# Optimization experiments

Hardware: AMD Instinct MI355X
Metric: run time of the kernel (lower is better)

Reference implementation:

```python
import jax, jax.numpy as jnp
import numpy as np

N_NODES = 50000
N_EDGES = 800000
DIM_IN = 128
DIM_H = 128
DIM_OUT = 10
N_GRAPHS = 256


def _glorot(key, shape):
    lim = float(np.sqrt(6.0 / (shape[0] + shape[1])))
    return jax.random.uniform(key, shape, jnp.float32, -lim, lim)


def setup_inputs() -> dict:
    key = jax.random.key(0)
    ks = jax.random.split(key, 8)
    x = jax.random.normal(ks[0], (N_NODES, DIM_IN), jnp.float32)
    edge_index = jax.random.randint(ks[1], (2, N_EDGES), 0, N_NODES, dtype=jnp.int64)
    batch = jnp.sort(jax.random.randint(ks[2], (N_NODES,), 0, N_GRAPHS, dtype=jnp.int64))
    return {
        'x': x,
        'edge_index': edge_index,
        'batch': batch,
        'W1': _glorot(ks[3], (DIM_IN, DIM_H)),
        'b1': jnp.zeros((DIM_H,), jnp.float32),
        'W2': _glorot(ks[4], (DIM_H, DIM_H)),
        'b2': jnp.zeros((DIM_H,), jnp.float32),
        'Wl1': _glorot(ks[5], (2 * DIM_H, 2 * DIM_H)),
        'bl1': jnp.zeros((2 * DIM_H,), jnp.float32),
        'Wl2': _glorot(ks[6], (2 * DIM_H, DIM_OUT)),
        'bl2': jnp.zeros((DIM_OUT,), jnp.float32),
    }


def _gcn_conv(h, W, b, src, dst, norm, n):
    # x @ W, gather source rows, scale by symmetric norm, scatter-add to dest
    m = (h @ W)[src] * norm[:, None]          # [E+N, dim_h]
    return jax.ops.segment_sum(m, dst, num_segments=n) + b


def reference(x, edge_index, batch, W1, b1, W2, b2, Wl1, bl1, Wl2, bl2):
    n = x.shape[0]
    loops = jnp.arange(n, dtype=edge_index.dtype)
    src = jnp.concatenate([edge_index[0], loops])  # add self-loops (PyG GCNConv default)
    dst = jnp.concatenate([edge_index[1], loops])
    deg = jax.ops.segment_sum(jnp.ones_like(dst, x.dtype), dst, num_segments=n)
    dinv = jnp.where(deg > 0, jax.lax.rsqrt(jnp.maximum(deg, 1.0)), 0.0)
    norm = dinv[src] * dinv[dst]
    # eval mode: dropout is identity
    h1 = _gcn_conv(x, W1, b1, src, dst, norm, n)
    h2 = _gcn_conv(h1, W2, b2, src, dst, norm, n)
    g1 = jax.ops.segment_sum(h1, batch, num_segments=N_GRAPHS)  # global_add_pool
    g2 = jax.ops.segment_sum(h2, batch, num_segments=N_GRAPHS)
    g = jnp.concatenate([g1, g2], axis=1)  # [N_GRAPHS, 2*dim_h]
    h = jax.nn.relu(g @ Wl1 + bl1)
    h = h @ Wl2 + bl2
    return (h, jax.nn.log_softmax(h, axis=1))
```

## Files before the change

### kernel.cpp

```cpp
#include <hip/hip_runtime.h>
#include <hip/hip_bf16.h>
#include <math.h>


#define DIMH 128
#define EBCAP 8192
#define SCAT_CHUNK 2048

typedef __attribute__((ext_vector_type(8))) short s16x8;
typedef __attribute__((ext_vector_type(4))) float f32x4;

__device__ inline ushort f2b(float f) {
    uint u = __float_as_uint(f);
    return (ushort)((u + 0x7fffu + ((u >> 16) & 1u)) >> 16);
}
__device__ inline uint pack2(float lo, float hi) {
    return (uint)f2b(lo) | ((uint)f2b(hi) << 16);
}
__device__ inline float blo(uint u) { return __uint_as_float(u << 16); }
__device__ inline float bhi(uint u) { return __uint_as_float(u & 0xffff0000u); }

__global__ __launch_bounds__(256) void k_front(const int* __restrict__ src,
                                               const int* __restrict__ dst,
                                               int* __restrict__ bcnt,
                                               uint* __restrict__ ebuf, int E, int scnb,
                                               const float* __restrict__ x,
                                               ushort* __restrict__ Xb, int n8, int cvnb,
                                               const float* __restrict__ W1,
                                               const float* __restrict__ W2,
                                               ushort* __restrict__ WT1,
                                               ushort* __restrict__ WT2) {
    __shared__ int h[4][256];
    __shared__ int wb[4][256];
    int blk = blockIdx.x;
    int t = threadIdx.x;
    if (blk < scnb) {
        int wave = t >> 6;
        h[0][t] = 0; h[1][t] = 0; h[2][t] = 0; h[3][t] = 0;
        __syncthreads();
        int e0 = blk * SCAT_CHUNK;
        int e1 = e0 + SCAT_CHUNK; if (e1 > E) e1 = E;
        for (int e = e0 + t; e < e1; e += 256)
            atomicAdd(&h[wave][dst[e] >> 8], 1);
        __syncthreads();
        {
            int h0 = h[0][t], h1 = h[1][t], h2 = h[2][t], h3 = h[3][t];
            int tot = h0 + h1 + h2 + h3;
            int gb = tot ? atomicAdd(&bcnt[t], tot) : 0;
            wb[0][t] = gb;
            wb[1][t] = gb + h0;
            wb[2][t] = gb + h0 + h1;
            wb[3][t] = gb + h0 + h1 + h2;
            h[0][t] = 0; h[1][t] = 0; h[2][t] = 0; h[3][t] = 0;
        }
        __syncthreads();
        for (int e = e0 + t; e < e1; e += 256) {
            int d = dst[e];
            int bk = d >> 8;
            int rank = wb[wave][bk] + atomicAdd(&h[wave][bk], 1);
            if (rank < EBCAP)
                ebuf[(size_t)bk * EBCAP + rank] = ((uint)(d & 255) << 24) | (uint)src[e];
        }
    } else if (blk < scnb + cvnb) {
        int i = (blk - scnb) * 256 + t;
        if (i < n8) {
            const float4* in4 = (const float4*)x;
            float4 a = in4[2 * i], b = in4[2 * i + 1];
            uint4 o;
            o.x = pack2(a.x, a.y); o.y = pack2(a.z, a.w);
            o.z = pack2(b.x, b.y); o.w = pack2(b.z, b.w);
            *(uint4*)(Xb + (size_t)i * 8) = o;
        }
    } else {
        int idx = (blk - scnb - cvnb) * 256 + t;
        const float* W = (idx < 16384) ? W1 : W2;
        ushort* WT = (idx < 16384) ? WT1 : WT2;
        int tt = idx & 16383;
        int k = tt >> 7, nn = tt & 127;
        WT[nn * 128 + k] = f2b(W[tt]);
    }
}

__global__ __launch_bounds__(256) void k_bcsr(const uint* __restrict__ ebuf,
                                              const int* __restrict__ bcnt,
                                              float* __restrict__ dinv,
                                              int2* __restrict__ rng,
                                              int* __restrict__ srt, int n) {
    __shared__ int cnt[256];
    __shared__ int wsum[4];
    __shared__ int stage[EBCAP];
    int b = blockIdx.x;
    int t = threadIdx.x;
    int c = bcnt[b]; if (c > EBCAP) c = EBCAP;
    size_t B = (size_t)b * EBCAP;
    cnt[t] = 0;
    __syncthreads();
    for (int i = t; i < c; i += 256)
        atomicAdd(&cnt[ebuf[B + i] >> 24], 1);
    __syncthreads();
    int v = cnt[t];
    int incl = v;
    for (int k = 1; k < 64; k <<= 1) {
        int u = __shfl_up(incl, k, 64);
        if ((t & 63) >= k) incl += u;
    }
    if ((t & 63) == 63) wsum[t >> 6] = incl;
    __syncthreads();
    int add = 0;
    for (int j = 0; j < (t >> 6); ++j) add += wsum[j];
    incl += add;
    int loc = incl - v;
    int node = b * 256 + t;
    if (node < n) {
        dinv[node] = rsqrtf((float)(v + 1));
        rng[node] = make_int2((int)B + loc, (int)B + loc + v);
    }
    cnt[t] = loc;
    __syncthreads();
    for (int i = t; i < c; i += 256) {
        uint r = ebuf[B + i];
        int p = atomicAdd(&cnt[r >> 24], 1);
        stage[p] = (int)(r & 0xffffffu);
    }
    __syncthreads();
    for (int i = t; i < c; i += 256) srt[B + i] = stage[i];
}

__device__ __forceinline__ void gemm_body(const ushort* __restrict__ Xb,
                                          const ushort* __restrict__ WT,
                                          const float* __restrict__ scale,
                                          ushort* __restrict__ P, int n,
                                          int blk, ushort* lds) {
    ushort* Xs = lds;
    ushort* Ws = lds + 64 * 128;
    const int tid = threadIdx.x;
    const int row0 = blk * 64;
    for (int ci = tid; ci < 1024; ci += 256) {
        int r = ci >> 4, c16 = ci & 15;
        uint dstB = (uint)(r * 256 + c16 * 16) ^ (uint)((r & 7) << 4);
        uint4 v = make_uint4(0u, 0u, 0u, 0u);
        if (row0 + r < n) v = *(const uint4*)(Xb + (size_t)(row0 + r) * 128 + c16 * 8);
        *(uint4*)((char*)Xs + dstB) = v;
    }
    for (int ci = tid; ci < 2048; ci += 256) {
        int r = ci >> 4, c16 = ci & 15;
        uint dstB = (uint)(r * 256 + c16 * 16) ^ (uint)((r & 7) << 4);
        *(uint4*)((char*)Ws + dstB) = *(const uint4*)(WT + (size_t)r * 128 + c16 * 8);
    }
    __syncthreads();
    const int wave = tid >> 6, lane = tid & 63;
    const int l15 = lane & 15, g = lane >> 4;
    f32x4 acc[8];
#pragma unroll
    for (int nt = 0; nt < 8; ++nt) acc[nt] = (f32x4){0.f, 0.f, 0.f, 0.f};
    const int tr = wave * 16 + l15;
    const uint aswz = (uint)((tr & 7) << 4);
#pragma unroll
    for (int kk = 0; kk < 4; ++kk) {
        uint aB = ((uint)(tr * 256 + kk * 64 + g * 16)) ^ aswz;
        s16x8 afrag = *(const s16x8*)((const char*)Xs + aB);
#pragma unroll
        for (int nt = 0; nt < 8; ++nt) {
            int wr = nt * 16 + l15;
            uint bB = ((uint)(wr * 256 + kk * 64 + g * 16)) ^ ((uint)((wr & 7) << 4));
            s16x8 bfrag = *(const s16x8*)((const char*)Ws + bB);
            acc[nt] = __builtin_amdgcn_mfma_f32_16x16x32_bf16(afrag, bfrag, acc[nt], 0, 0, 0);
        }
    }
    float sc[4];
#pragma unroll
    for (int reg = 0; reg < 4; ++reg) {
        int grow = row0 + wave * 16 + g * 4 + reg;
        sc[reg] = (grow < n) ? scale[grow] : 0.f;
    }
#pragma unroll
    for (int nt = 0; nt < 8; ++nt) {
        int gcol = nt * 16 + l15;
#pragma unroll
        for (int reg = 0; reg < 4; ++reg) {
            int grow = row0 + wave * 16 + g * 4 + reg;
            if (grow < n) P[(size_t)grow * 128 + gcol] = f2b(sc[reg] * acc[nt][reg]);
        }
    }
}

__global__ __launch_bounds__(256) void k_gemm(const ushort* __restrict__ Xb,
                                              const ushort* __restrict__ WT,
                                              const float* __restrict__ scale,
                                              ushort* __restrict__ P, int n) {
    __shared__ ushort lds[64 * 128 + 128 * 128];
    gemm_body(Xb, WT, scale, P, n, blockIdx.x, lds);
}

__device__ __forceinline__ void pool_body(const ushort* __restrict__ Hb,
                                          const int* __restrict__ batch,
                                          float* __restrict__ Gpart, int n,
                                          int blk, int* range, float* part) {
    int g = blk >> 2, q = blk & 3;
    if (threadIdx.x < 2) {
        int target = g + threadIdx.x;
        int lo = 0, hi = n;
        while (lo < hi) { int m = (lo + hi) >> 1; if (batch[m] < target) lo = m + 1; else hi = m; }
        range[threadIdx.x] = lo;
    }
    __syncthreads();
    int c = threadIdx.x & 127, h = threadIdx.x >> 7;
    int r = range[0] + q * 2 + h, r1 = range[1];
    float s0 = 0.f, s1 = 0.f;
    for (; r + 8 < r1; r += 16) {
        s0 += __uint_as_float((uint)Hb[(size_t)r       * 128 + c] << 16);
        s1 += __uint_as_float((uint)Hb[(size_t)(r + 8) * 128 + c] << 16);
    }
    for (; r < r1; r += 8) s0 += __uint_as_float((uint)Hb[(size_t)r * 128 + c] << 16);
    part[threadIdx.x] = s0 + s1;
    __syncthreads();
    if (threadIdx.x < 128)
        Gpart[(size_t)blk * 128 + threadIdx.x] = part[threadIdx.x] + part[threadIdx.x + 128];
}

__global__ __launch_bounds__(256) void k_mid(const ushort* __restrict__ Hb,
                                             const ushort* __restrict__ WT,
                                             const float* __restrict__ scale,
                                             ushort* __restrict__ P, int n, int gemnb,
                                             const int* __restrict__ batch,
                                             float* __restrict__ Gpart) {
    __shared__ ushort lds[64 * 128 + 128 * 128];
    __shared__ int range[2];
    __shared__ float part[256];
    int blk = blockIdx.x;
    if (blk < gemnb) {
        gemm_body(Hb, WT, scale, P, n, blk, lds);
    } else {
        pool_body(Hb, batch, Gpart, n, blk - gemnb, range, part);
    }
}

__global__ __launch_bounds__(256) void k_aggregate(const ushort* __restrict__ Pb,
                                                   const int2* __restrict__ rng,
                                                   const int* __restrict__ srt,
                                                   const float* __restrict__ dinv,
                                                   const float* __restrict__ bias,
                                                   ushort* __restrict__ Hb, int n) {
    int wave = threadIdx.x >> 6;
    int lane = threadIdx.x & 63;
    int i = blockIdx.x * 4 + wave;
    if (i >= n) return;
    int q   = lane >> 4;
    int sub = lane & 15;
    const uint4* P4 = (const uint4*)Pb;
    float a0 = 0.f, a1 = 0.f, a2 = 0.f, a3 = 0.f;
    float a4 = 0.f, a5 = 0.f, a6 = 0.f, a7 = 0.f;
    if (q == 0) {
        uint4 u = P4[(size_t)i * 16 + sub];
        a0 = blo(u.x); a1 = bhi(u.x); a2 = blo(u.y); a3 = bhi(u.y);
        a4 = blo(u.z); a5 = bhi(u.z); a6 = blo(u.w); a7 = bhi(u.w);
    }
    int2 r2 = rng[i];
    int e1 = r2.y;
    int e  = r2.x + q;
    while (e + 12 < e1) {
        int s0 = srt[e], s1 = srt[e + 4], s2 = srt[e + 8], s3 = srt[e + 12];
        uint4 u0 = P4[(size_t)s0 * 16 + sub];
        uint4 u1 = P4[(size_t)s1 * 16 + sub];
        uint4 u2 = P4[(size_t)s2 * 16 + sub];
        uint4 u3 = P4[(size_t)s3 * 16 + sub];
        a0 += (blo(u0.x) + blo(u1.x)) + (blo(u2.x) + blo(u3.x));
        a1 += (bhi(u0.x) + bhi(u1.x)) + (bhi(u2.x) + bhi(u3.x));
        a2 += (blo(u0.y) + blo(u1.y)) + (blo(u2.y) + blo(u3.y));
        a3 += (bhi(u0.y) + bhi(u1.y)) + (bhi(u2.y) + bhi(u3.y));
        a4 += (blo(u0.z) + blo(u1.z)) + (blo(u2.z) + blo(u3.z));
        a5 += (bhi(u0.z) + bhi(u1.z)) + (bhi(u2.z) + bhi(u3.z));
        a6 += (blo(u0.w) + blo(u1.w)) + (blo(u2.w) + blo(u3.w));
        a7 += (bhi(u0.w) + bhi(u1.w)) + (bhi(u2.w) + bhi(u3.w));
        e += 16;
    }
    while (e < e1) {
        uint4 u = P4[(size_t)srt[e] * 16 + sub];
        a0 += blo(u.x); a1 += bhi(u.x); a2 += blo(u.y); a3 += bhi(u.y);
        a4 += blo(u.z); a5 += bhi(u.z); a6 += blo(u.w); a7 += bhi(u.w);
        e += 4;
    }
    a0 += __shfl_xor(a0, 16, 64); a0 += __shfl_xor(a0, 32, 64);
    a1 += __shfl_xor(a1, 16, 64); a1 += __shfl_xor(a1, 32, 64);
    a2 += __shfl_xor(a2, 16, 64); a2 += __shfl_xor(a2, 32, 64);
    a3 += __shfl_xor(a3, 16, 64); a3 += __shfl_xor(a3, 32, 64);
    a4 += __shfl_xor(a4, 16, 64); a4 += __shfl_xor(a4, 32, 64);
    a5 += __shfl_xor(a5, 16, 64); a5 += __shfl_xor(a5, 32, 64);
    a6 += __shfl_xor(a6, 16, 64); a6 += __shfl_xor(a6, 32, 64);
    a7 += __shfl_xor(a7, 16, 64); a7 += __shfl_xor(a7, 32, 64);
    if (q == 0) {
        float di = dinv[i];
        int c = sub * 8;
        float4 b0 = *(const float4*)(bias + c);
        float4 b1 = *(const float4*)(bias + c + 4);
        uint4 o;
        o.x = pack2(fmaf(di, a0, b0.x), fmaf(di, a1, b0.y));
        o.y = pack2(fmaf(di, a2, b0.z), fmaf(di, a3, b0.w));
        o.z = pack2(fmaf(di, a4, b1.x), fmaf(di, a5, b1.y));
        o.w = pack2(fmaf(di, a6, b1.z), fmaf(di, a7, b1.w));
        *(uint4*)(Hb + (size_t)i * 128 + c) = o;
    }
}

__global__ __launch_bounds__(256) void k_mlp(const float* __restrict__ Gp1,
                                             const ushort* __restrict__ Hb,
                                             const int* __restrict__ batch, int n,
                                             const float* __restrict__ Wl1,
                                             const float* __restrict__ bl1,
                                             const float* __restrict__ Wl2,
                                             const float* __restrict__ bl2,
                                             float* __restrict__ out) {
    __shared__ float gs[256];
    __shared__ float zs[256];
    __shared__ float part[256];
    __shared__ float l[10];
    __shared__ int range[2];
    int g = blockIdx.x, j = threadIdx.x;
    if (j < 2) {
        int target = g + j;
        int lo = 0, hi = n;
        while (lo < hi) { int m = (lo + hi) >> 1; if (batch[m] < target) lo = m + 1; else hi = m; }
        range[j] = lo;
    }
    __syncthreads();
    {
        int c = j & 127, h = j >> 7;
        int r = range[0] + h, r1 = range[1];
        float s0 = 0.f, s1 = 0.f, s2 = 0.f, s3 = 0.f;
        for (; r + 6 < r1; r += 8) {
            s0 += __uint_as_float((uint)Hb[(size_t)r       * 128 + c] << 16);
            s1 += __uint_as_float((uint)Hb[(size_t)(r + 2) * 128 + c] << 16);
            s2 += __uint_as_float((uint)Hb[(size_t)(r + 4) * 128 + c] << 16);
            s3 += __uint_as_float((uint)Hb[(size_t)(r + 6) * 128 + c] << 16);
        }
        for (; r < r1; r += 2) s0 += __uint_as_float((uint)Hb[(size_t)r * 128 + c] << 16);
        part[j] = (s0 + s1) + (s2 + s3);
    }
    __syncthreads();
    if (j < 128) {
        const float* p = Gp1 + (size_t)g * 512 + j;
        gs[j] = (p[0] + p[128]) + (p[256] + p[384]);
        gs[128 + j] = part[j] + part[j + 128];
    }
    __syncthreads();
    float acc = bl1[j];
    for (int k = 0; k < 256; ++k) acc = fmaf(gs[k], Wl1[k * 256 + j], acc);
    zs[j] = fmaxf(acc, 0.f);
    __syncthreads();
    if (j < 10) {
        float a = bl2[j];
        for (int k = 0; k < 256; ++k) a = fmaf(zs[k], Wl2[k * 10 + j], a);
        l[j] = a;
    }
    __syncthreads();
    if (j < 10) {
        float m = l[0];
        for (int i = 1; i < 10; ++i) m = fmaxf(m, l[i]);
        float s = 0.f;
        for (int i = 0; i < 10; ++i) s += expf(l[i] - m);
        float lse = m + logf(s);
        out[g * 10 + j] = l[j];
        out[2560 + g * 10 + j] = l[j] - lse;
    }
}

static inline size_t alignup(size_t v) { return (v + 255) & ~(size_t)255; }

extern "C" void kernel_launch(void* const* d_in, const int* in_sizes, int n_in,
                              void* d_out, int out_size, void* d_ws, size_t ws_size,
                              hipStream_t stream) {
    const float* x    = (const float*)d_in[0];
    const int*   edge = (const int*)d_in[1];
    const int*   batch= (const int*)d_in[2];
    const float* W1   = (const float*)d_in[3];
    const float* b1   = (const float*)d_in[4];
    const float* W2   = (const float*)d_in[5];
    const float* b2   = (const float*)d_in[6];
    const float* Wl1  = (const float*)d_in[7];
    const float* bl1  = (const float*)d_in[8];
    const float* Wl2  = (const float*)d_in[9];
    const float* bl2  = (const float*)d_in[10];

    const int N = in_sizes[2];
    const int E = in_sizes[1] / 2;
    const int* srcIdx = edge;
    const int* dstIdx = edge + E;

    const int nb = (N + 255) >> 8;

    char* ws = (char*)d_ws;
    ushort* Xb    = (ushort*)ws; ws += alignup((size_t)N * DIMH * 2);
    ushort* P     = (ushort*)ws; ws += alignup((size_t)N * DIMH * 2);
    ushort* Hb    = (ushort*)ws; ws += alignup((size_t)N * DIMH * 2);
    ushort* WT1   = (ushort*)ws; ws += alignup((size_t)128 * 128 * 2);
    ushort* WT2   = (ushort*)ws; ws += alignup((size_t)128 * 128 * 2);
    float*  dinv  = (float*)ws;  ws += alignup((size_t)N * 4);
    int2*   rng   = (int2*)ws;   ws += alignup((size_t)N * 8);
    int*    srt   = (int*)ws;    ws += alignup((size_t)nb * EBCAP * 4);
    uint*   ebuf  = (uint*)ws;   ws += alignup((size_t)nb * EBCAP * 4);
    int*    bcnt  = (int*)ws;    ws += alignup((size_t)256 * 4);
    float*  Gp1   = (float*)ws;  ws += alignup((size_t)1024 * 128 * 4);

    const int scnb  = (E + SCAT_CHUNK - 1) / SCAT_CHUNK;
    const int n8    = N * DIMH / 8;
    const int cvnb  = (n8 + 255) / 256;
    const int gemnb = (N + 63) / 64;
    const int aggnb = (N + 3) / 4;

    hipMemsetAsync(bcnt, 0, (size_t)256 * 4, stream);
    k_front<<<scnb + cvnb + 128, 256, 0, stream>>>(srcIdx, dstIdx, bcnt, ebuf, E, scnb,
                                                   x, Xb, n8, cvnb, W1, W2, WT1, WT2);
    k_bcsr<<<nb, 256, 0, stream>>>(ebuf, bcnt, dinv, rng, srt, N);
    k_gemm<<<gemnb, 256, 0, stream>>>(Xb, WT1, dinv, P, N);
    k_aggregate<<<aggnb, 256, 0, stream>>>(P, rng, srt, dinv, b1, Hb, N);
    k_mid<<<gemnb + 1024, 256, 0, stream>>>(Hb, WT2, dinv, P, N, gemnb, batch, Gp1);
    k_aggregate<<<aggnb, 256, 0, stream>>>(P, rng, srt, dinv, b2, Hb, N);
    k_mlp<<<256, 256, 0, stream>>>(Gp1, Hb, batch, N, Wl1, bl1, Wl2, bl2, (float*)d_out);
}
```

Before: 179.6 us.

## Fuse x conversion into first GEMM and merge it with CSR build kernel

The separate fp32-to-bf16 conversion of x is removed, and the first GEMM now reads fp32 x directly and packs it into LDS. Because the GEMM no longer applies the source-side dinv scale, it can run in the same launch as the CSR-building blocks, cutting one kernel launch and one full pass over a bf16 copy of x. In exchange, the aggregation now gathers dinv[src] per edge and multiplies it in with FMAs, which adds scattered 4-byte loads to the edge loop.

```diff
diff --git a/kernel.cpp b/kernel.cpp
--- a/kernel.cpp
+++ b/kernel.cpp
@@ -24,8 +24,6 @@
                                                const int* __restrict__ dst,
                                                int* __restrict__ bcnt,
                                                uint* __restrict__ ebuf, int E, int scnb,
-                                               const float* __restrict__ x,
-                                               ushort* __restrict__ Xb, int n8, int cvnb,
                                                const float* __restrict__ W1,
                                                const float* __restrict__ W2,
                                                ushort* __restrict__ WT1,
@@ -61,18 +59,8 @@
             if (rank < EBCAP)
                 ebuf[(size_t)bk * EBCAP + rank] = ((uint)(d & 255) << 24) | (uint)src[e];
         }
-    } else if (blk < scnb + cvnb) {
-        int i = (blk - scnb) * 256 + t;
-        if (i < n8) {
-            const float4* in4 = (const float4*)x;
-            float4 a = in4[2 * i], b = in4[2 * i + 1];
-            uint4 o;
-            o.x = pack2(a.x, a.y); o.y = pack2(a.z, a.w);
-            o.z = pack2(b.x, b.y); o.w = pack2(b.z, b.w);
-            *(uint4*)(Xb + (size_t)i * 8) = o;
-        }
     } else {
-        int idx = (blk - scnb - cvnb) * 256 + t;
+        int idx = (blk - scnb) * 256 + t;
         const float* W = (idx < 16384) ? W1 : W2;
         ushort* WT = (idx < 16384) ? WT1 : WT2;
         int tt = idx & 16383;
@@ -81,15 +69,12 @@
     }
 }
 
-__global__ __launch_bounds__(256) void k_bcsr(const uint* __restrict__ ebuf,
-                                              const int* __restrict__ bcnt,
-                                              float* __restrict__ dinv,
-                                              int2* __restrict__ rng,
-                                              int* __restrict__ srt, int n) {
-    __shared__ int cnt[256];
-    __shared__ int wsum[4];
-    __shared__ int stage[EBCAP];
-    int b = blockIdx.x;
+__device__ __forceinline__ void bcsr_body(const uint* __restrict__ ebuf,
+                                          const int* __restrict__ bcnt,
+                                          float* __restrict__ dinv,
+                                          int2* __restrict__ rng,
+                                          int* __restrict__ srt, int n,
+                                          int b, int* cnt, int* wsum, int* stage) {
     int t = threadIdx.x;
     int c = bcnt[b]; if (c > EBCAP) c = EBCAP;
     size_t B = (size_t)b * EBCAP;
@@ -126,21 +111,36 @@
     for (int i = t; i < c; i += 256) srt[B + i] = stage[i];
 }
 
-__device__ __forceinline__ void gemm_body(const ushort* __restrict__ Xb,
+template<bool F32IN>
+__device__ __forceinline__ void gemm_body(const void* __restrict__ Xin,
                                           const ushort* __restrict__ WT,
-                                          const float* __restrict__ scale,
                                           ushort* __restrict__ P, int n,
                                           int blk, ushort* lds) {
     ushort* Xs = lds;
     ushort* Ws = lds + 64 * 128;
     const int tid = threadIdx.x;
     const int row0 = blk * 64;
-    for (int ci = tid; ci < 1024; ci += 256) {
-        int r = ci >> 4, c16 = ci & 15;
-        uint dstB = (uint)(r * 256 + c16 * 16) ^ (uint)((r & 7) << 4);
-        uint4 v = make_uint4(0u, 0u, 0u, 0u);
-        if (row0 + r < n) v = *(const uint4*)(Xb + (size_t)(row0 + r) * 128 + c16 * 8);
-        *(uint4*)((char*)Xs + dstB) = v;
+    if (F32IN) {
+        const float* Xf = (const float*)Xin;
+        for (int ci = tid; ci < 2048; ci += 256) {
+            int r = ci >> 5, c8 = ci & 31;
+            uint dstB = (uint)(r * 256 + c8 * 8) ^ (uint)((r & 7) << 4);
+            uint2 v = make_uint2(0u, 0u);
+            if (row0 + r < n) {
+                float4 f = *(const float4*)(Xf + (size_t)(row0 + r) * 128 + c8 * 4);
+                v.x = pack2(f.x, f.y); v.y = pack2(f.z, f.w);
+            }
+            *(uint2*)((char*)Xs + dstB) = v;
+        }
+    } else {
+        const ushort* Xb = (const ushort*)Xin;
+        for (int ci = tid; ci < 1024; ci += 256) {
+            int r = ci >> 4, c16 = ci & 15;
+            uint dstB = (uint)(r * 256 + c16 * 16) ^ (uint)((r & 7) << 4);
+            uint4 v = make_uint4(0u, 0u, 0u, 0u);
+            if (row0 + r < n) v = *(const uint4*)(Xb + (size_t)(row0 + r) * 128 + c16 * 8);
+            *(uint4*)((char*)Xs + dstB) = v;
+        }
     }
     for (int ci = tid; ci < 2048; ci += 256) {
         int r = ci >> 4, c16 = ci & 15;
@@ -167,29 +167,35 @@
             acc[nt] = __builtin_amdgcn_mfma_f32_16x16x32_bf16(afrag, bfrag, acc[nt], 0, 0, 0);
         }
     }
-    float sc[4];
-#pragma unroll
-    for (int reg = 0; reg < 4; ++reg) {
-        int grow = row0 + wave * 16 + g * 4 + reg;
-        sc[reg] = (grow < n) ? scale[grow] : 0.f;
-    }
 #pragma unroll
     for (int nt = 0; nt < 8; ++nt) {
         int gcol = nt * 16 + l15;
 #pragma unroll
         for (int reg = 0; reg < 4; ++reg) {
             int grow = row0 + wave * 16 + g * 4 + reg;
-            if (grow < n) P[(size_t)grow * 128 + gcol] = f2b(sc[reg] * acc[nt][reg]);
-        }
-    }
-}
-
-__global__ __launch_bounds__(256) void k_gemm(const ushort* __restrict__ Xb,
-                                              const ushort* __restrict__ WT,
-                                              const float* __restrict__ scale,
-                                              ushort* __restrict__ P, int n) {
+            if (grow < n) P[(size_t)grow * 128 + gcol] = f2b(acc[nt][reg]);
+        }
+    }
+}
+
+__global__ __launch_bounds__(256) void k_g1csr(const float* __restrict__ x,
+                                               const ushort* __restrict__ WT1,
+                                               ushort* __restrict__ P, int n, int gemnb,
+                                               const uint* __restrict__ ebuf,
+                                               const int* __restrict__ bcnt,
+                                               float* __restrict__ dinv,
+                                               int2* __restrict__ rng,
+                                               int* __restrict__ srt) {
     __shared__ ushort lds[64 * 128 + 128 * 128];
-    gemm_body(Xb, WT, scale, P, n, blockIdx.x, lds);
+    int blk = blockIdx.x;
+    if (blk < gemnb) {
+        gemm_body<true>(x, WT1, P, n, blk, lds);
+    } else {
+        int* cnt   = (int*)lds;
+        int* wsum  = cnt + 256;
+        int* stage = wsum + 8;
+        bcsr_body(ebuf, bcnt, dinv, rng, srt, n, blk - gemnb, cnt, wsum, stage);
+    }
 }
 
 __device__ __forceinline__ void pool_body(const ushort* __restrict__ Hb,
@@ -220,7 +226,6 @@
 
 __global__ __launch_bounds__(256) void k_mid(const ushort* __restrict__ Hb,
                                              const ushort* __restrict__ WT,
-                                             const float* __restrict__ scale,
                                              ushort* __restrict__ P, int n, int gemnb,
                                              const int* __restrict__ batch,
                                              float* __restrict__ Gpart) {
@@ -229,7 +234,7 @@
     __shared__ float part[256];
     int blk = blockIdx.x;
     if (blk < gemnb) {
-        gemm_body(Hb, WT, scale, P, n, blk, lds);
+        gemm_body<false>(Hb, WT, P, n, blk, lds);
     } else {
         pool_body(Hb, batch, Gpart, n, blk - gemnb, range, part);
     }
@@ -248,36 +253,42 @@
     int q   = lane >> 4;
     int sub = lane & 15;
     const uint4* P4 = (const uint4*)Pb;
+    float di = dinv[i];
     float a0 = 0.f, a1 = 0.f, a2 = 0.f, a3 = 0.f;
     float a4 = 0.f, a5 = 0.f, a6 = 0.f, a7 = 0.f;
     if (q == 0) {
         uint4 u = P4[(size_t)i * 16 + sub];
-        a0 = blo(u.x); a1 = bhi(u.x); a2 = blo(u.y); a3 = bhi(u.y);
-        a4 = blo(u.z); a5 = bhi(u.z); a6 = blo(u.w); a7 = bhi(u.w);
+        a0 = di * blo(u.x); a1 = di * bhi(u.x); a2 = di * blo(u.y); a3 = di * bhi(u.y);
+        a4 = di * blo(u.z); a5 = di * bhi(u.z); a6 = di * blo(u.w); a7 = di * bhi(u.w);
     }
     int2 r2 = rng[i];
     int e1 = r2.y;
     int e  = r2.x + q;
     while (e + 12 < e1) {
         int s0 = srt[e], s1 = srt[e + 4], s2 = srt[e + 8], s3 = srt[e + 12];
+        float d0 = dinv[s0], d1 = dinv[s1], d2 = dinv[s2], d3 = dinv[s3];
         uint4 u0 = P4[(size_t)s0 * 16 + sub];
         uint4 u1 = P4[(size_t)s1 * 16 + sub];
         uint4 u2 = P4[(size_t)s2 * 16 + sub];
         uint4 u3 = P4[(size_t)s3 * 16 + sub];
-        a0 += (blo(u0.x) + blo(u1.x)) + (blo(u2.x) + blo(u3.x));
-        a1 += (bhi(u0.x) + bhi(u1.x)) + (bhi(u2.x) + bhi(u3.x));
-        a2 += (blo(u0.y) + blo(u1.y)) + (blo(u2.y) + blo(u3.y));
-        a3 += (bhi(u0.y) + bhi(u1.y)) + (bhi(u2.y) + bhi(u3.y));
-        a4 += (blo(u0.z) + blo(u1.z)) + (blo(u2.z) + blo(u3.z));
-        a5 += (bhi(u0.z) + bhi(u1.z)) + (bhi(u2.z) + bhi(u3.z));
-        a6 += (blo(u0.w) + blo(u1.w)) + (blo(u2.w) + blo(u3.w));
-        a7 += (bhi(u0.w) + bhi(u1.w)) + (bhi(u2.w) + bhi(u3.w));
+        a0 = fmaf(d0, blo(u0.x), fmaf(d1, blo(u1.x), fmaf(d2, blo(u2.x), fmaf(d3, blo(u3.x), a0))));
+        a1 = fmaf(d0, bhi(u0.x), fmaf(d1, bhi(u1.x), fmaf(d2, bhi(u2.x), fmaf(d3, bhi(u3.x), a1))));
+        a2 = fmaf(d0, blo(u0.y), fmaf(d1, blo(u1.y), fmaf(d2, blo(u2.y), fmaf(d3, blo(u3.y), a2))));
+        a3 = fmaf(d0, bhi(u0.y), fmaf(d1, bhi(u1.y), fmaf(d2, bhi(u2.y), fmaf(d3, bhi(u3.y), a3))));
+        a4 = fmaf(d0, blo(u0.z), fmaf(d1, blo(u1.z), fmaf(d2, blo(u2.z), fmaf(d3, blo(u3.z), a4))));
+        a5 = fmaf(d0, bhi(u0.z), fmaf(d1, bhi(u1.z), fmaf(d2, bhi(u2.z), fmaf(d3, bhi(u3.z), a5))));
+        a6 = fmaf(d0, blo(u0.w), fmaf(d1, blo(u1.w), fmaf(d2, blo(u2.w), fmaf(d3, blo(u3.w), a6))));
+        a7 = fmaf(d0, bhi(u0.w), fmaf(d1, bhi(u1.w), fmaf(d2, bhi(u2.w), fmaf(d3, bhi(u3.w), a7))));
         e += 16;
     }
     while (e < e1) {
-        uint4 u = P4[(size_t)srt[e] * 16 + sub];
-        a0 += blo(u.x); a1 += bhi(u.x); a2 += blo(u.y); a3 += bhi(u.y);
-        a4 += blo(u.z); a5 += bhi(u.z); a6 += blo(u.w); a7 += bhi(u.w);
+        int s = srt[e];
+        float ds = dinv[s];
+        uint4 u = P4[(size_t)s * 16 + sub];
+        a0 = fmaf(ds, blo(u.x), a0); a1 = fmaf(ds, bhi(u.x), a1);
+        a2 = fmaf(ds, blo(u.y), a2); a3 = fmaf(ds, bhi(u.y), a3);
+        a4 = fmaf(ds, blo(u.z), a4); a5 = fmaf(ds, bhi(u.z), a5);
+        a6 = fmaf(ds, blo(u.w), a6); a7 = fmaf(ds, bhi(u.w), a7);
         e += 4;
     }
     a0 += __shfl_xor(a0, 16, 64); a0 += __shfl_xor(a0, 32, 64);
@@ -289,7 +300,6 @@
     a6 += __shfl_xor(a6, 16, 64); a6 += __shfl_xor(a6, 32, 64);
     a7 += __shfl_xor(a7, 16, 64); a7 += __shfl_xor(a7, 32, 64);
     if (q == 0) {
-        float di = dinv[i];
         int c = sub * 8;
         float4 b0 = *(const float4*)(bias + c);
         float4 b1 = *(const float4*)(bias + c + 4);
@@ -389,7 +399,6 @@
     const int nb = (N + 255) >> 8;
 
     char* ws = (char*)d_ws;
-    ushort* Xb    = (ushort*)ws; ws += alignup((size_t)N * DIMH * 2);
     ushort* P     = (ushort*)ws; ws += alignup((size_t)N * DIMH * 2);
     ushort* Hb    = (ushort*)ws; ws += alignup((size_t)N * DIMH * 2);
     ushort* WT1   = (ushort*)ws; ws += alignup((size_t)128 * 128 * 2);
@@ -402,18 +411,16 @@
     float*  Gp1   = (float*)ws;  ws += alignup((size_t)1024 * 128 * 4);
 
     const int scnb  = (E + SCAT_CHUNK - 1) / SCAT_CHUNK;
-    const int n8    = N * DIMH / 8;
-    const int cvnb  = (n8 + 255) / 256;
     const int gemnb = (N + 63) / 64;
     const int aggnb = (N + 3) / 4;
 
     hipMemsetAsync(bcnt, 0, (size_t)256 * 4, stream);
-    k_front<<<scnb + cvnb + 128, 256, 0, stream>>>(srcIdx, dstIdx, bcnt, ebuf, E, scnb,
-                                                   x, Xb, n8, cvnb, W1, W2, WT1, WT2);
-    k_bcsr<<<nb, 256, 0, stream>>>(ebuf, bcnt, dinv, rng, srt, N);
-    k_gemm<<<gemnb, 256, 0, stream>>>(Xb, WT1, dinv, P, N);
+    k_front<<<scnb + 128, 256, 0, stream>>>(srcIdx, dstIdx, bcnt, ebuf, E, scnb,
+                                            W1, W2, WT1, WT2);
+    k_g1csr<<<gemnb + nb, 256, 0, stream>>>(x, WT1, P, N, gemnb,
+                                            ebuf, bcnt, dinv, rng, srt);
     k_aggregate<<<aggnb, 256, 0, stream>>>(P, rng, srt, dinv, b1, Hb, N);
-    k_mid<<<gemnb + 1024, 256, 0, stream>>>(Hb, WT2, dinv, P, N, gemnb, batch, Gp1);
+    k_mid<<<gemnb + 1024, 256, 0, stream>>>(Hb, WT2, P, N, gemnb, batch, Gp1);
     k_aggregate<<<aggnb, 256, 0, stream>>>(P, rng, srt, dinv, b2, Hb, N);
     k_mlp<<<256, 256, 0, stream>>>(Gp1, Hb, batch, N, Wl1, bl1, Wl2, bl2, (float*)d_out);
 }
```

Measured after the change: 164.2 us. 1.09x faster.
